# Optimization experiments

Measured on AMD Instinct MI355X. Metric: run time of the kernel, lower is better.

The kernel has to match this reference:

```python
import jax, jax.numpy as jnp
import numpy as np

N = 150000   # nodes
E = 600000   # edges
F_IN = 32    # node features
H = 128      # hidden_channels == MLP_neurons
G = 2048     # graphs in batch


def setup_inputs() -> dict:
    key = jax.random.key(0)
    ks = iter(jax.random.split(key, 40))
    inp = {}
    inp['x'] = jax.random.normal(next(ks), (N, F_IN), dtype=jnp.float32)
    inp['edge_index'] = jax.random.randint(next(ks), (2, E), 0, N)
    inp['batch'] = jnp.sort(jax.random.randint(next(ks), (N,), 0, G))
    # GINConv MLPs: Linear(in,H) ReLU Linear(H,H) ReLU Linear(H,H)
    for i, f_in in enumerate([F_IN, H, H]):
        s1 = 1.0 / np.sqrt(f_in)
        s2 = 1.0 / np.sqrt(H)
        inp[f'c{i}_w1'] = jax.random.uniform(next(ks), (f_in, H), minval=-s1, maxval=s1)
        inp[f'c{i}_b1'] = jnp.zeros((H,), jnp.float32)
        inp[f'c{i}_w2'] = jax.random.uniform(next(ks), (H, H), minval=-s2, maxval=s2)
        inp[f'c{i}_b2'] = jnp.zeros((H,), jnp.float32)
        inp[f'c{i}_w3'] = jax.random.uniform(next(ks), (H, H), minval=-s2, maxval=s2)
        inp[f'c{i}_b3'] = jnp.zeros((H,), jnp.float32)
    s = 1.0 / np.sqrt(H)
    inp['fc0_w'] = jax.random.uniform(next(ks), (H, H), minval=-s, maxval=s)
    inp['fc0_b'] = jnp.zeros((H,), jnp.float32)
    inp['fc1_w'] = jax.random.uniform(next(ks), (H, H), minval=-s, maxval=s)
    inp['fc1_b'] = jnp.zeros((H,), jnp.float32)
    inp['out_w'] = jax.random.uniform(next(ks), (H, 2), minval=-s, maxval=s)
    inp['out_b'] = jnp.zeros((2,), jnp.float32)
    return inp


def _gin_layer(x, edge_index, w1, b1, w2, b2, w3, b3):
    # GINConv with eps=0: h = MLP(x + sum_{j in N(i)} x_j)
    agg = jax.ops.segment_sum(x[edge_index[0]], edge_index[1], num_segments=N)
    h = x + agg
    h = jax.nn.relu(h @ w1 + b1)
    h = jax.nn.relu(h @ w2 + b2)
    h = h @ w3 + b3
    return jax.nn.relu(h)  # outer .relu() in forward


def reference(x, edge_index, batch,
              c0_w1, c0_b1, c0_w2, c0_b2, c0_w3, c0_b3,
              c1_w1, c1_b1, c1_w2, c1_b2, c1_w3, c1_b3,
              c2_w1, c2_b1, c2_w2, c2_b2, c2_w3, c2_b3,
              fc0_w, fc0_b, fc1_w, fc1_b, out_w, out_b):
    h = _gin_layer(x, edge_index, c0_w1, c0_b1, c0_w2, c0_b2, c0_w3, c0_b3)
    h = _gin_layer(h, edge_index, c1_w1, c1_b1, c1_w2, c1_b2, c1_w3, c1_b3)
    h = _gin_layer(h, edge_index, c2_w1, c2_b1, c2_w2, c2_b2, c2_w3, c2_b3)
    # global_mean_pool over graph ids
    sums = jax.ops.segment_sum(h, batch, num_segments=G)            # [G,H]
    cnts = jax.ops.segment_sum(jnp.ones((N,), h.dtype), batch, num_segments=G)
    g = sums / jnp.maximum(cnts, 1.0)[:, None]
    # classifier head (dropout is identity at inference)
    g = jax.nn.relu(g @ fc0_w + fc0_b)
    g = jax.nn.relu(g @ fc1_w + fc1_b)
    return g @ out_w + out_b  # [G,2]
```

## Files before the change

kernel.cpp:

```cpp
#include <hip/hip_runtime.h>
#include <hip/hip_bf16.h>

#define NN 150000
#define EE 600000
#define F_IN 32
#define HD 128
#define GG 2048
#define CAP 28
#define NP 150016

typedef __attribute__((ext_vector_type(8))) short bf16x8;
typedef __attribute__((ext_vector_type(4))) float f32x4;

__device__ inline void split_bf16(float v, unsigned short& hi, unsigned short& lo) {
    __hip_bfloat16 h = __float2bfloat16(v);
    float hv = __bfloat162float(h);
    __hip_bfloat16 l = __float2bfloat16(v - hv);
    hi = *reinterpret_cast<unsigned short*>(&h);
    lo = *reinterpret_cast<unsigned short*>(&l);
}
__device__ inline unsigned short bf16_hi(float v) {
    __hip_bfloat16 h = __float2bfloat16(v);
    return *reinterpret_cast<unsigned short*>(&h);
}
__device__ inline unsigned short bf16_lo(float v) {
    __hip_bfloat16 h = __float2bfloat16(v);
    float hv = __bfloat162float(h);
    __hip_bfloat16 l = __float2bfloat16(v - hv);
    return *reinterpret_cast<unsigned short*>(&l);
}
__device__ inline float bf2f(unsigned short u) {
    union { unsigned int i; float f; } c;
    c.i = ((unsigned int)u) << 16;
    return c.f;
}

__global__ void build_graph(const int* __restrict__ ei,
                            int* __restrict__ cnt_node,
                            int* __restrict__ bucket) {
    int e = blockIdx.x * blockDim.x + threadIdx.x;
    if (e >= EE) return;
    int src = ei[e];
    int dst = ei[EE + e];
    int slot = atomicAdd(&cnt_node[dst], 1);
    if (slot < CAP) bucket[slot * NN + dst] = src;
}

struct PrepDesc { const float* src; unsigned short* dhi; unsigned short* dlo; int K; };
struct PrepArgs { PrepDesc d[9]; };

__global__ void prep_weights(PrepArgs pa) {
    PrepDesc de = pa.d[blockIdx.y];
    int total = de.K * HD;
    int KS = de.K >> 5;
    for (int idx = blockIdx.x * blockDim.x + threadIdx.x; idx < total;
         idx += gridDim.x * blockDim.x) {
        int k = idx / HD, h = idx - (idx / HD) * HD;
        unsigned short hi, lo;
        split_bf16(de.src[idx], hi, lo);
        int nt = h >> 4, m = h & 15;
        int ks = k >> 5, quad = (k >> 3) & 3, e = k & 7;
        int lane = quad * 16 + m;
        int pidx = ((nt * KS + ks) * 64 + lane) * 8 + e;
        de.dhi[pidx] = hi;
        de.dlo[pidx] = lo;
    }
}

template <int K_IN, bool BF16IN, bool POOL>
__launch_bounds__(256, 3)
__global__ void gin_layer(const void* __restrict__ hin_,
                          const int* __restrict__ cnt_node,
                          const int* __restrict__ bucket,
                          const unsigned short* __restrict__ w1h, const unsigned short* __restrict__ w1l,
                          const float* __restrict__ b1,
                          const unsigned short* __restrict__ w2h, const unsigned short* __restrict__ w2l,
                          const float* __restrict__ b2,
                          const unsigned short* __restrict__ w3h, const unsigned short* __restrict__ w3l,
                          const float* __restrict__ b3,
                          unsigned short* __restrict__ out,
                          const int* __restrict__ batch,
                          float* __restrict__ pooled) {
    constexpr int KS1 = K_IN / 32;
    constexpr int UN = BF16IN ? 4 : (KS1 == 1 ? 8 : 2);
    __shared__ unsigned short sh[4][32][HD + 8];

    const int wave = threadIdx.x >> 6;
    const int lane = threadIdx.x & 63;
    const int m = lane & 15;
    const int quad = lane >> 4;
    const int nodeBase = blockIdx.x * 128 + wave * 32;

    const float* hf = (const float*)hin_;
    const unsigned short* hb = (const unsigned short*)hin_;

    bf16x8 ah[2][KS1], al[2][KS1];
#pragma unroll
    for (int s = 0; s < 2; s++) {
        int node = nodeBase + s * 16 + m;
        node = node < NN ? node : NN - 1;
        float ag[KS1][8];
        if (BF16IN) {
            const unsigned short* rs = hb + (size_t)node * K_IN + quad * 8;
#pragma unroll
            for (int ks = 0; ks < KS1; ks++) {
                bf16x8 v = *(const bf16x8*)(rs + ks * 32);
#pragma unroll
                for (int e = 0; e < 8; e++) ag[ks][e] = bf2f((unsigned short)v[e]);
            }
        } else {
            const float* rs = hf + (size_t)node * K_IN + quad * 8;
#pragma unroll
            for (int ks = 0; ks < KS1; ks++) {
                float4 v0 = *(const float4*)(rs + ks * 32);
                float4 v1 = *(const float4*)(rs + ks * 32 + 4);
                ag[ks][0] = v0.x; ag[ks][1] = v0.y; ag[ks][2] = v0.z; ag[ks][3] = v0.w;
                ag[ks][4] = v1.x; ag[ks][5] = v1.y; ag[ks][6] = v1.z; ag[ks][7] = v1.w;
            }
        }
        int cnt = cnt_node[node];
        cnt = cnt < CAP ? cnt : CAP;
        const int* b = bucket + node;
        int i = 0;
        if (BF16IN) {
            for (; i + UN <= cnt; i += UN) {
                bf16x8 v[UN][KS1];
#pragma unroll
                for (int j = 0; j < UN; j++) {
                    const unsigned short* r = hb + (size_t)b[(i + j) * NN] * K_IN + quad * 8;
#pragma unroll
                    for (int ks = 0; ks < KS1; ks++)
                        v[j][ks] = *(const bf16x8*)(r + ks * 32);
                }
#pragma unroll
                for (int ks = 0; ks < KS1; ks++)
#pragma unroll
                    for (int e = 0; e < 8; e++) {
                        float t01 = bf2f((unsigned short)v[0][ks][e]) +
                                    bf2f((unsigned short)v[1][ks][e]);
                        float t23 = bf2f((unsigned short)v[2][ks][e]) +
                                    bf2f((unsigned short)v[3][ks][e]);
                        ag[ks][e] += t01 + t23;
                    }
            }
            for (; i < cnt; i++) {
                const unsigned short* r = hb + (size_t)b[i * NN] * K_IN + quad * 8;
#pragma unroll
                for (int ks = 0; ks < KS1; ks++) {
                    bf16x8 v = *(const bf16x8*)(r + ks * 32);
#pragma unroll
                    for (int e = 0; e < 8; e++) ag[ks][e] += bf2f((unsigned short)v[e]);
                }
            }
        } else {
            for (; i + UN <= cnt; i += UN) {
                float4 v0[UN][KS1], v1[UN][KS1];
#pragma unroll
                for (int j = 0; j < UN; j++) {
                    const float* r = hf + (size_t)b[(i + j) * NN] * K_IN + quad * 8;
#pragma unroll
                    for (int ks = 0; ks < KS1; ks++) {
                        v0[j][ks] = *(const float4*)(r + ks * 32);
                        v1[j][ks] = *(const float4*)(r + ks * 32 + 4);
                    }
                }
#pragma unroll
                for (int ks = 0; ks < KS1; ks++) {
#pragma unroll
                    for (int e = 0; e < 4; e++) {
                        float s01 = (&v0[0][ks].x)[e] + (&v0[1][ks].x)[e];
                        float s23 = (&v0[2][ks].x)[e] + (&v0[3][ks].x)[e];
                        if (UN == 8) {
                            s01 += (&v0[4][ks].x)[e] + (&v0[5][ks].x)[e];
                            s23 += (&v0[6][ks].x)[e] + (&v0[7][ks].x)[e];
                        }
                        ag[ks][e] += s01 + s23;
                    }
#pragma unroll
                    for (int e = 0; e < 4; e++) {
                        float s01 = (&v1[0][ks].x)[e] + (&v1[1][ks].x)[e];
                        float s23 = (&v1[2][ks].x)[e] + (&v1[3][ks].x)[e];
                        if (UN == 8) {
                            s01 += (&v1[4][ks].x)[e] + (&v1[5][ks].x)[e];
                            s23 += (&v1[6][ks].x)[e] + (&v1[7][ks].x)[e];
                        }
                        ag[ks][e + 4] += s01 + s23;
                    }
                }
            }
            for (; i < cnt; i++) {
                const float* r = hf + (size_t)b[i * NN] * K_IN + quad * 8;
#pragma unroll
                for (int ks = 0; ks < KS1; ks++) {
                    float4 v0 = *(const float4*)(r + ks * 32);
                    float4 v1 = *(const float4*)(r + ks * 32 + 4);
                    ag[ks][0] += v0.x; ag[ks][1] += v0.y; ag[ks][2] += v0.z; ag[ks][3] += v0.w;
                    ag[ks][4] += v1.x; ag[ks][5] += v1.y; ag[ks][6] += v1.z; ag[ks][7] += v1.w;
                }
            }
        }
#pragma unroll
        for (int ks = 0; ks < KS1; ks++) {
            bf16x8 vh, vl;
#pragma unroll
            for (int e = 0; e < 8; e++) {
                unsigned short hi, lo;
                split_bf16(ag[ks][e], hi, lo);
                vh[e] = (short)hi;
                vl[e] = (short)lo;
            }
            ah[s][ks] = vh;
            al[s][ks] = vl;
        }
    }

    f32x4 acc[2][8];

#pragma unroll
    for (int nt = 0; nt < 8; nt++) {
        bf16x8 bh[KS1], bl[KS1];
#pragma unroll
        for (int ks = 0; ks < KS1; ks++) {
            bh[ks] = *(const bf16x8*)(w1h + ((nt * KS1 + ks) * 64 + lane) * 8);
            bl[ks] = *(const bf16x8*)(w1l + ((nt * KS1 + ks) * 64 + lane) * 8);
        }
        f32x4 c0 = {0.f, 0.f, 0.f, 0.f};
        f32x4 c1 = {0.f, 0.f, 0.f, 0.f};
#pragma unroll
        for (int ks = 0; ks < KS1; ks++) {
            c0 = __builtin_amdgcn_mfma_f32_16x16x32_bf16(ah[0][ks], bh[ks], c0, 0, 0, 0);
            c1 = __builtin_amdgcn_mfma_f32_16x16x32_bf16(ah[1][ks], bh[ks], c1, 0, 0, 0);
            c0 = __builtin_amdgcn_mfma_f32_16x16x32_bf16(al[0][ks], bh[ks], c0, 0, 0, 0);
            c1 = __builtin_amdgcn_mfma_f32_16x16x32_bf16(al[1][ks], bh[ks], c1, 0, 0, 0);
            c0 = __builtin_amdgcn_mfma_f32_16x16x32_bf16(ah[0][ks], bl[ks], c0, 0, 0, 0);
            c1 = __builtin_amdgcn_mfma_f32_16x16x32_bf16(ah[1][ks], bl[ks], c1, 0, 0, 0);
        }
        acc[0][nt] = c0;
        acc[1][nt] = c1;
    }

    bf16x8 a2h[2][4], a2l[2][4];
#pragma unroll
    for (int s = 0; s < 2; s++)
#pragma unroll
        for (int nt = 0; nt < 8; nt++) {
            float bj = b1[nt * 16 + m];
#pragma unroll
            for (int r = 0; r < 4; r++)
                sh[wave][s * 16 + quad * 4 + r][nt * 16 + m] =
                    bf16_hi(fmaxf(acc[s][nt][r] + bj, 0.f));
        }
#pragma unroll
    for (int s = 0; s < 2; s++)
#pragma unroll
        for (int ks = 0; ks < 4; ks++)
            a2h[s][ks] = *(const bf16x8*)&sh[wave][s * 16 + m][ks * 32 + quad * 8];
#pragma unroll
    for (int s = 0; s < 2; s++)
#pragma unroll
        for (int nt = 0; nt < 8; nt++) {
            float bj = b1[nt * 16 + m];
#pragma unroll
            for (int r = 0; r < 4; r++)
                sh[wave][s * 16 + quad * 4 + r][nt * 16 + m] =
                    bf16_lo(fmaxf(acc[s][nt][r] + bj, 0.f));
        }
#pragma unroll
    for (int s = 0; s < 2; s++)
#pragma unroll
        for (int ks = 0; ks < 4; ks++)
            a2l[s][ks] = *(const bf16x8*)&sh[wave][s * 16 + m][ks * 32 + quad * 8];

#pragma unroll
    for (int nt = 0; nt < 8; nt++) {
        bf16x8 bh[4], bl[4];
#pragma unroll
        for (int ks = 0; ks < 4; ks++) {
            bh[ks] = *(const bf16x8*)(w2h + ((nt * 4 + ks) * 64 + lane) * 8);
            bl[ks] = *(const bf16x8*)(w2l + ((nt * 4 + ks) * 64 + lane) * 8);
        }
        f32x4 c0 = {0.f, 0.f, 0.f, 0.f};
        f32x4 c1 = {0.f, 0.f, 0.f, 0.f};
#pragma unroll
        for (int ks = 0; ks < 4; ks++) {
            c0 = __builtin_amdgcn_mfma_f32_16x16x32_bf16(a2h[0][ks], bh[ks], c0, 0, 0, 0);
            c1 = __builtin_amdgcn_mfma_f32_16x16x32_bf16(a2h[1][ks], bh[ks], c1, 0, 0, 0);
            c0 = __builtin_amdgcn_mfma_f32_16x16x32_bf16(a2l[0][ks], bh[ks], c0, 0, 0, 0);
            c1 = __builtin_amdgcn_mfma_f32_16x16x32_bf16(a2l[1][ks], bh[ks], c1, 0, 0, 0);
            c0 = __builtin_amdgcn_mfma_f32_16x16x32_bf16(a2h[0][ks], bl[ks], c0, 0, 0, 0);
            c1 = __builtin_amdgcn_mfma_f32_16x16x32_bf16(a2h[1][ks], bl[ks], c1, 0, 0, 0);
        }
        acc[0][nt] = c0;
        acc[1][nt] = c1;
    }

#pragma unroll
    for (int s = 0; s < 2; s++)
#pragma unroll
        for (int nt = 0; nt < 8; nt++) {
            float bj = b2[nt * 16 + m];
#pragma unroll
            for (int r = 0; r < 4; r++)
                sh[wave][s * 16 + quad * 4 + r][nt * 16 + m] =
                    bf16_hi(fmaxf(acc[s][nt][r] + bj, 0.f));
        }
#pragma unroll
    for (int s = 0; s < 2; s++)
#pragma unroll
        for (int ks = 0; ks < 4; ks++)
            a2h[s][ks] = *(const bf16x8*)&sh[wave][s * 16 + m][ks * 32 + quad * 8];
#pragma unroll
    for (int s = 0; s < 2; s++)
#pragma unroll
        for (int nt = 0; nt < 8; nt++) {
            float bj = b2[nt * 16 + m];
#pragma unroll
            for (int r = 0; r < 4; r++)
                sh[wave][s * 16 + quad * 4 + r][nt * 16 + m] =
                    bf16_lo(fmaxf(acc[s][nt][r] + bj, 0.f));
        }
#pragma unroll
    for (int s = 0; s < 2; s++)
#pragma unroll
        for (int ks = 0; ks < 4; ks++)
            a2l[s][ks] = *(const bf16x8*)&sh[wave][s * 16 + m][ks * 32 + quad * 8];

#pragma unroll
    for (int nt = 0; nt < 8; nt++) {
        bf16x8 bh[4], bl[4];
#pragma unroll
        for (int ks = 0; ks < 4; ks++) {
            bh[ks] = *(const bf16x8*)(w3h + ((nt * 4 + ks) * 64 + lane) * 8);
            bl[ks] = *(const bf16x8*)(w3l + ((nt * 4 + ks) * 64 + lane) * 8);
        }
        f32x4 c0 = {0.f, 0.f, 0.f, 0.f};
        f32x4 c1 = {0.f, 0.f, 0.f, 0.f};
#pragma unroll
        for (int ks = 0; ks < 4; ks++) {
            c0 = __builtin_amdgcn_mfma_f32_16x16x32_bf16(a2h[0][ks], bh[ks], c0, 0, 0, 0);
            c1 = __builtin_amdgcn_mfma_f32_16x16x32_bf16(a2h[1][ks], bh[ks], c1, 0, 0, 0);
            c0 = __builtin_amdgcn_mfma_f32_16x16x32_bf16(a2l[0][ks], bh[ks], c0, 0, 0, 0);
            c1 = __builtin_amdgcn_mfma_f32_16x16x32_bf16(a2l[1][ks], bh[ks], c1, 0, 0, 0);
            c0 = __builtin_amdgcn_mfma_f32_16x16x32_bf16(a2h[0][ks], bl[ks], c0, 0, 0, 0);
            c1 = __builtin_amdgcn_mfma_f32_16x16x32_bf16(a2h[1][ks], bl[ks], c1, 0, 0, 0);
        }
        acc[0][nt] = c0;
        acc[1][nt] = c1;
    }

    if (POOL) {
        float* shf = (float*)&sh[wave][0][0];
#pragma unroll
        for (int h = 0; h < 2; h++) {
#pragma unroll
            for (int nt = 0; nt < 8; nt++) {
                float bj = b3[nt * 16 + m];
#pragma unroll
                for (int r = 0; r < 4; r++)
                    shf[(quad * 4 + r) * 132 + nt * 16 + m] =
                        fmaxf(acc[h][nt][r] + bj, 0.f);
            }
            int c0 = lane * 2;
            float run0 = 0.f, run1 = 0.f;
            int gp = -1;
            for (int rrow = 0; rrow < 16; rrow++) {
                int node = nodeBase + h * 16 + rrow;
                if (node >= NN) break;
                int g = batch[node];
                float2 xv = *(const float2*)&shf[rrow * 132 + c0];
                if (g != gp) {
                    if (gp >= 0) {
                        atomicAdd(&pooled[(size_t)gp * HD + c0 + 0], run0);
                        atomicAdd(&pooled[(size_t)gp * HD + c0 + 1], run1);
                    }
                    run0 = xv.x; run1 = xv.y; gp = g;
                } else {
                    run0 += xv.x; run1 += xv.y;
                }
            }
            if (gp >= 0) {
                atomicAdd(&pooled[(size_t)gp * HD + c0 + 0], run0);
                atomicAdd(&pooled[(size_t)gp * HD + c0 + 1], run1);
            }
        }
    } else {
#pragma unroll
        for (int s = 0; s < 2; s++)
#pragma unroll
            for (int nt = 0; nt < 8; nt++) {
                float bj = b3[nt * 16 + m];
#pragma unroll
                for (int r = 0; r < 4; r++)
                    sh[wave][s * 16 + quad * 4 + r][nt * 16 + m] =
                        bf16_hi(fmaxf(acc[s][nt][r] + bj, 0.f));
            }
#pragma unroll
        for (int io = 0; io < 8; io++) {
            int row32 = io * 4 + quad;
            int col = m * 8;
            int n2 = nodeBase + row32;
            bf16x8 v = *(const bf16x8*)&sh[wave][row32][col];
            if (n2 < NN) *(bf16x8*)&out[(size_t)n2 * HD + col] = v;
        }
    }
}

__device__ inline int lb_batch(const int* __restrict__ batch, int key) {
    int lo = 0, hi = NN;
    while (lo < hi) {
        int mid = (lo + hi) >> 1;
        if (batch[mid] < key) lo = mid + 1; else hi = mid;
    }
    return lo;
}

__launch_bounds__(128)
__global__ void head(const float* __restrict__ pooled, const int* __restrict__ batch,
                     const float* __restrict__ fc0_w, const float* __restrict__ fc0_b,
                     const float* __restrict__ fc1_w, const float* __restrict__ fc1_b,
                     const float* __restrict__ out_w, const float* __restrict__ out_b,
                     float* __restrict__ out) {
    int g = blockIdx.x;
    int j = threadIdx.x;
    __shared__ float s0[HD];
    __shared__ float s1[HD];
    int c = lb_batch(batch, g + 1) - lb_batch(batch, g);
    float cf = (float)(c > 1 ? c : 1);
    s0[j] = pooled[(size_t)g * HD + j] / cf;
    __syncthreads();

    float acc = fc0_b[j];
    for (int k = 0; k < HD; k += 4) {
        float4 hv = *(const float4*)&s0[k];
        acc = fmaf(hv.x, fc0_w[(k + 0) * HD + j], acc);
        acc = fmaf(hv.y, fc0_w[(k + 1) * HD + j], acc);
        acc = fmaf(hv.z, fc0_w[(k + 2) * HD + j], acc);
        acc = fmaf(hv.w, fc0_w[(k + 3) * HD + j], acc);
    }
    s1[j] = fmaxf(acc, 0.0f);
    __syncthreads();

    acc = fc1_b[j];
    for (int k = 0; k < HD; k += 4) {
        float4 hv = *(const float4*)&s1[k];
        acc = fmaf(hv.x, fc1_w[(k + 0) * HD + j], acc);
        acc = fmaf(hv.y, fc1_w[(k + 1) * HD + j], acc);
        acc = fmaf(hv.z, fc1_w[(k + 2) * HD + j], acc);
        acc = fmaf(hv.w, fc1_w[(k + 3) * HD + j], acc);
    }
    float v = fmaxf(acc, 0.0f);

    float p0 = v * out_w[j * 2 + 0];
    float p1 = v * out_w[j * 2 + 1];
    __syncthreads();
    s0[j] = p0;
    s1[j] = p1;
    __syncthreads();
    for (int off = 64; off >= 1; off >>= 1) {
        if (j < off) {
            s0[j] += s0[j + off];
            s1[j] += s1[j + off];
        }
        __syncthreads();
    }
    if (j == 0) {
        out[(size_t)g * 2 + 0] = s0[0] + out_b[0];
        out[(size_t)g * 2 + 1] = s1[0] + out_b[1];
    }
}

extern "C" void kernel_launch(void* const* d_in, const int* in_sizes, int n_in,
                              void* d_out, int out_size, void* d_ws, size_t ws_size,
                              hipStream_t stream) {
    const float* x     = (const float*)d_in[0];
    const int*   ei    = (const int*)d_in[1];
    const int*   batch = (const int*)d_in[2];
    const float* cw[3][6];
    for (int i = 0; i < 3; i++)
        for (int k = 0; k < 6; k++) cw[i][k] = (const float*)d_in[3 + 6 * i + k];
    const float* fc0_w = (const float*)d_in[21];
    const float* fc0_b = (const float*)d_in[22];
    const float* fc1_w = (const float*)d_in[23];
    const float* fc1_b = (const float*)d_in[24];
    const float* out_w = (const float*)d_in[25];
    const float* out_b = (const float*)d_in[26];
    float* out = (float*)d_out;

    char* ws = (char*)d_ws;
    size_t off = 0;
    auto carve = [&](size_t bytes) {
        void* p = ws + off;
        off += (bytes + 255) & ~(size_t)255;
        return p;
    };
    int*   cnt_node = (int*)carve((size_t)NN * 4);
    float* pooled   = (float*)carve((size_t)GG * HD * 4);
    int*   bucket   = (int*)carve((size_t)NN * CAP * 4);
    unsigned short* hA = (unsigned short*)carve((size_t)NP * HD * 2);
    unsigned short* hB = (unsigned short*)carve((size_t)NP * HD * 2);
    unsigned short* wHi[9];
    unsigned short* wLo[9];
    int wK[9] = {F_IN, HD, HD, HD, HD, HD, HD, HD, HD};
    for (int i = 0; i < 9; i++) {
        wHi[i] = (unsigned short*)carve((size_t)wK[i] * HD * 2);
        wLo[i] = (unsigned short*)carve((size_t)wK[i] * HD * 2);
    }
    (void)ws_size;

    hipMemsetAsync(cnt_node, 0, (size_t)((char*)bucket - (char*)cnt_node), stream);
    build_graph<<<(EE + 255) / 256, 256, 0, stream>>>(ei, cnt_node, bucket);

    PrepArgs pa;
    for (int l = 0; l < 3; l++)
        for (int s = 0; s < 3; s++) {
            int i = l * 3 + s;
            pa.d[i].src = cw[l][2 * s];
            pa.d[i].dhi = wHi[i];
            pa.d[i].dlo = wLo[i];
            pa.d[i].K = wK[i];
        }
    prep_weights<<<dim3(16, 9), 256, 0, stream>>>(pa);

    const int blocks = NP / 128;

    gin_layer<F_IN, false, false><<<blocks, 256, 0, stream>>>(x, cnt_node, bucket,
        wHi[0], wLo[0], cw[0][1], wHi[1], wLo[1], cw[0][3], wHi[2], wLo[2], cw[0][5],
        hA, batch, pooled);
    gin_layer<HD, true, false><<<blocks, 256, 0, stream>>>(hA, cnt_node, bucket,
        wHi[3], wLo[3], cw[1][1], wHi[4], wLo[4], cw[1][3], wHi[5], wLo[5], cw[1][5],
        hB, batch, pooled);
    gin_layer<HD, true, true><<<blocks, 256, 0, stream>>>(hB, cnt_node, bucket,
        wHi[6], wLo[6], cw[2][1], wHi[7], wLo[7], cw[2][3], wHi[8], wLo[8], cw[2][5],
        nullptr, batch, pooled);

    head<<<GG, 128, 0, stream>>>(pooled, batch, fc0_w, fc0_b, fc1_w, fc1_b, out_w, out_b, out);
}
```

Baseline: 520.5 us.

## Split neighbor aggregation into separate wave-per-node-group kernels before MLP

Each GIN layer becomes two kernels. A dedicated aggregation kernel has one wave handle four nodes, with lanes spread across feature dimensions and neighbor indices broadcast by shuffle. It writes the summed features as hi/lo bf16 planes that the MLP kernel reads directly. The bucket layout changes to node-major so a node's neighbor list is contiguous, and the memset is replaced by a zeroing kernel. This trades the fused kernel's poorly coalesced per-lane gather and low occupancy for extra global round trips of the aggregated tensors and more launches.

```diff
diff --git a/kernel.cpp b/kernel.cpp
--- a/kernel.cpp
+++ b/kernel.cpp
@@ -33,6 +33,17 @@
     union { unsigned int i; float f; } c;
     c.i = ((unsigned int)u) << 16;
     return c.f;
+}
+__device__ inline float asfloat(unsigned int u) {
+    union { unsigned int i; float f; } c;
+    c.i = u;
+    return c.f;
+}
+
+__global__ void init_zero(int* __restrict__ cnt_node, float* __restrict__ pooled) {
+    int i = blockIdx.x * blockDim.x + threadIdx.x;
+    if (i < NN) cnt_node[i] = 0;
+    if (i < GG * HD) pooled[i] = 0.f;
 }
 
 __global__ void build_graph(const int* __restrict__ ei,
@@ -43,7 +54,7 @@
     int src = ei[e];
     int dst = ei[EE + e];
     int slot = atomicAdd(&cnt_node[dst], 1);
-    if (slot < CAP) bucket[slot * NN + dst] = src;
+    if (slot < CAP) bucket[dst * CAP + slot] = src;
 }
 
 struct PrepDesc { const float* src; unsigned short* dhi; unsigned short* dlo; int K; };
@@ -67,22 +78,157 @@
     }
 }
 
-template <int K_IN, bool BF16IN, bool POOL>
-__launch_bounds__(256, 3)
-__global__ void gin_layer(const void* __restrict__ hin_,
-                          const int* __restrict__ cnt_node,
-                          const int* __restrict__ bucket,
-                          const unsigned short* __restrict__ w1h, const unsigned short* __restrict__ w1l,
-                          const float* __restrict__ b1,
-                          const unsigned short* __restrict__ w2h, const unsigned short* __restrict__ w2l,
-                          const float* __restrict__ b2,
-                          const unsigned short* __restrict__ w3h, const unsigned short* __restrict__ w3l,
-                          const float* __restrict__ b3,
-                          unsigned short* __restrict__ out,
-                          const int* __restrict__ batch,
-                          float* __restrict__ pooled) {
+__launch_bounds__(256, 8)
+__global__ void agg_b16(const unsigned short* __restrict__ hb,
+                        const int* __restrict__ cnt_node,
+                        const int* __restrict__ bucket,
+                        unsigned short* __restrict__ aggH,
+                        unsigned short* __restrict__ aggL) {
+    const int wave = threadIdx.x >> 6;
+    const int lane = threadIdx.x & 63;
+    const int nbase = (blockIdx.x * 4 + wave) * 4;
+    if (nbase >= NN) return;
+
+    int cv = cnt_node[min(nbase + (lane & 3), NN - 1)];
+    int tots[4];
+#pragma unroll
+    for (int i = 0; i < 4; i++) {
+        int c = __shfl(cv, i);
+        c = c < CAP ? c : CAP;
+        tots[i] = (nbase + i < NN) ? c + 1 : 0;
+    }
+    int idxv[4];
+#pragma unroll
+    for (int i = 0; i < 4; i++) {
+        int n = min(nbase + i, NN - 1);
+        int slot = (lane >= 1 && lane <= CAP) ? lane - 1 : 0;
+        int bv = bucket[n * CAP + slot];
+        idxv[i] = (lane == 0) ? n : bv;
+    }
+    int mtot = max(max(tots[0], tots[1]), max(tots[2], tots[3]));
+
+    float a0[4] = {0.f, 0.f, 0.f, 0.f};
+    float a1[4] = {0.f, 0.f, 0.f, 0.f};
+
+    int j = 0;
+    while (j < mtot) {
+        unsigned int v[4][2];
+#pragma unroll
+        for (int i = 0; i < 4; i++)
+#pragma unroll
+            for (int jj = 0; jj < 2; jj++) {
+                v[i][jj] = 0u;
+                if (j + jj < tots[i]) {
+                    int sidx = __shfl(idxv[i], j + jj);
+                    v[i][jj] = *(const unsigned int*)(hb + (size_t)sidx * HD + lane * 2);
+                }
+            }
+#pragma unroll
+        for (int i = 0; i < 4; i++)
+#pragma unroll
+            for (int jj = 0; jj < 2; jj++) {
+                a0[i] += asfloat(v[i][jj] << 16);
+                a1[i] += asfloat(v[i][jj] & 0xffff0000u);
+            }
+        j += 2;
+    }
+
+#pragma unroll
+    for (int i = 0; i < 4; i++) {
+        if (nbase + i >= NN) break;
+        unsigned short h0, l0, h1, l1;
+        split_bf16(a0[i], h0, l0);
+        split_bf16(a1[i], h1, l1);
+        unsigned int ph = (unsigned int)h0 | ((unsigned int)h1 << 16);
+        unsigned int pl = (unsigned int)l0 | ((unsigned int)l1 << 16);
+        *(unsigned int*)(aggH + (size_t)(nbase + i) * HD + lane * 2) = ph;
+        *(unsigned int*)(aggL + (size_t)(nbase + i) * HD + lane * 2) = pl;
+    }
+}
+
+__launch_bounds__(256, 8)
+__global__ void agg_f32(const float* __restrict__ x,
+                        const int* __restrict__ cnt_node,
+                        const int* __restrict__ bucket,
+                        unsigned short* __restrict__ aggH,
+                        unsigned short* __restrict__ aggL) {
+    const int wave = threadIdx.x >> 6;
+    const int lane = threadIdx.x & 63;
+    const int half = lane >> 5;
+    const int dim = lane & 31;
+    const int nbase = (blockIdx.x * 4 + wave) * 4;
+    if (nbase >= NN) return;
+
+    int cv = cnt_node[min(nbase + (lane & 3), NN - 1)];
+    int tots[4];
+#pragma unroll
+    for (int i = 0; i < 4; i++) {
+        int c = __shfl(cv, i);
+        c = c < CAP ? c : CAP;
+        tots[i] = (nbase + i < NN) ? c + 1 : 0;
+    }
+    int idxv[4];
+#pragma unroll
+    for (int i = 0; i < 4; i++) {
+        int n = min(nbase + i, NN - 1);
+        int slot = (lane >= 1 && lane <= CAP) ? lane - 1 : 0;
+        int bv = bucket[n * CAP + slot];
+        idxv[i] = (lane == 0) ? n : bv;
+    }
+    int mtot = max(max(tots[0], tots[1]), max(tots[2], tots[3]));
+
+    float a[4] = {0.f, 0.f, 0.f, 0.f};
+
+    int j = 0;
+    while (j < mtot) {
+        float v[4][2], w[4][2];
+#pragma unroll
+        for (int i = 0; i < 4; i++)
+#pragma unroll
+            for (int p = 0; p < 2; p++) {
+                v[i][p] = 0.f; w[i][p] = 0.f;
+                int jb = j + p * 2;
+                if (jb < tots[i]) {
+                    int jj = jb + half;
+                    bool ok = jj < tots[i];
+                    int sidx = __shfl(idxv[i], ok ? jj : jb);
+                    v[i][p] = x[(size_t)sidx * F_IN + dim];
+                    w[i][p] = ok ? 1.f : 0.f;
+                }
+            }
+#pragma unroll
+        for (int i = 0; i < 4; i++)
+#pragma unroll
+            for (int p = 0; p < 2; p++)
+                a[i] = fmaf(v[i][p], w[i][p], a[i]);
+        j += 4;
+    }
+#pragma unroll
+    for (int i = 0; i < 4; i++) a[i] += __shfl_xor(a[i], 32);
+
+#pragma unroll
+    for (int i = 0; i < 4; i++) {
+        if (nbase + i >= NN) break;
+        unsigned short outv = half ? bf16_lo(a[i]) : bf16_hi(a[i]);
+        unsigned short* p = (half ? aggL : aggH) + (size_t)(nbase + i) * F_IN + dim;
+        *p = outv;
+    }
+}
+
+template <int K_IN, bool POOL>
+__launch_bounds__(256, 4)
+__global__ void gin_mlp(const unsigned short* __restrict__ aggH,
+                        const unsigned short* __restrict__ aggL,
+                        const unsigned short* __restrict__ w1h, const unsigned short* __restrict__ w1l,
+                        const float* __restrict__ b1,
+                        const unsigned short* __restrict__ w2h, const unsigned short* __restrict__ w2l,
+                        const float* __restrict__ b2,
+                        const unsigned short* __restrict__ w3h, const unsigned short* __restrict__ w3l,
+                        const float* __restrict__ b3,
+                        unsigned short* __restrict__ out,
+                        const int* __restrict__ batch,
+                        float* __restrict__ pooled) {
     constexpr int KS1 = K_IN / 32;
-    constexpr int UN = BF16IN ? 4 : (KS1 == 1 ? 8 : 2);
     __shared__ unsigned short sh[4][32][HD + 8];
 
     const int wave = threadIdx.x >> 6;
@@ -91,126 +237,17 @@
     const int quad = lane >> 4;
     const int nodeBase = blockIdx.x * 128 + wave * 32;
 
-    const float* hf = (const float*)hin_;
-    const unsigned short* hb = (const unsigned short*)hin_;
-
     bf16x8 ah[2][KS1], al[2][KS1];
 #pragma unroll
     for (int s = 0; s < 2; s++) {
         int node = nodeBase + s * 16 + m;
         node = node < NN ? node : NN - 1;
-        float ag[KS1][8];
-        if (BF16IN) {
-            const unsigned short* rs = hb + (size_t)node * K_IN + quad * 8;
-#pragma unroll
-            for (int ks = 0; ks < KS1; ks++) {
-                bf16x8 v = *(const bf16x8*)(rs + ks * 32);
-#pragma unroll
-                for (int e = 0; e < 8; e++) ag[ks][e] = bf2f((unsigned short)v[e]);
-            }
-        } else {
-            const float* rs = hf + (size_t)node * K_IN + quad * 8;
-#pragma unroll
-            for (int ks = 0; ks < KS1; ks++) {
-                float4 v0 = *(const float4*)(rs + ks * 32);
-                float4 v1 = *(const float4*)(rs + ks * 32 + 4);
-                ag[ks][0] = v0.x; ag[ks][1] = v0.y; ag[ks][2] = v0.z; ag[ks][3] = v0.w;
-                ag[ks][4] = v1.x; ag[ks][5] = v1.y; ag[ks][6] = v1.z; ag[ks][7] = v1.w;
-            }
-        }
-        int cnt = cnt_node[node];
-        cnt = cnt < CAP ? cnt : CAP;
-        const int* b = bucket + node;
-        int i = 0;
-        if (BF16IN) {
-            for (; i + UN <= cnt; i += UN) {
-                bf16x8 v[UN][KS1];
-#pragma unroll
-                for (int j = 0; j < UN; j++) {
-                    const unsigned short* r = hb + (size_t)b[(i + j) * NN] * K_IN + quad * 8;
-#pragma unroll
-                    for (int ks = 0; ks < KS1; ks++)
-                        v[j][ks] = *(const bf16x8*)(r + ks * 32);
-                }
-#pragma unroll
-                for (int ks = 0; ks < KS1; ks++)
-#pragma unroll
-                    for (int e = 0; e < 8; e++) {
-                        float t01 = bf2f((unsigned short)v[0][ks][e]) +
-                                    bf2f((unsigned short)v[1][ks][e]);
-                        float t23 = bf2f((unsigned short)v[2][ks][e]) +
-                                    bf2f((unsigned short)v[3][ks][e]);
-                        ag[ks][e] += t01 + t23;
-                    }
-            }
-            for (; i < cnt; i++) {
-                const unsigned short* r = hb + (size_t)b[i * NN] * K_IN + quad * 8;
-#pragma unroll
-                for (int ks = 0; ks < KS1; ks++) {
-                    bf16x8 v = *(const bf16x8*)(r + ks * 32);
-#pragma unroll
-                    for (int e = 0; e < 8; e++) ag[ks][e] += bf2f((unsigned short)v[e]);
-                }
-            }
-        } else {
-            for (; i + UN <= cnt; i += UN) {
-                float4 v0[UN][KS1], v1[UN][KS1];
-#pragma unroll
-                for (int j = 0; j < UN; j++) {
-                    const float* r = hf + (size_t)b[(i + j) * NN] * K_IN + quad * 8;
-#pragma unroll
-                    for (int ks = 0; ks < KS1; ks++) {
-                        v0[j][ks] = *(const float4*)(r + ks * 32);
-                        v1[j][ks] = *(const float4*)(r + ks * 32 + 4);
-                    }
-                }
-#pragma unroll
-                for (int ks = 0; ks < KS1; ks++) {
-#pragma unroll
-                    for (int e = 0; e < 4; e++) {
-                        float s01 = (&v0[0][ks].x)[e] + (&v0[1][ks].x)[e];
-                        float s23 = (&v0[2][ks].x)[e] + (&v0[3][ks].x)[e];
-                        if (UN == 8) {
-                            s01 += (&v0[4][ks].x)[e] + (&v0[5][ks].x)[e];
-                            s23 += (&v0[6][ks].x)[e] + (&v0[7][ks].x)[e];
-                        }
-                        ag[ks][e] += s01 + s23;
-                    }
-#pragma unroll
-                    for (int e = 0; e < 4; e++) {
-                        float s01 = (&v1[0][ks].x)[e] + (&v1[1][ks].x)[e];
-                        float s23 = (&v1[2][ks].x)[e] + (&v1[3][ks].x)[e];
-                        if (UN == 8) {
-                            s01 += (&v1[4][ks].x)[e] + (&v1[5][ks].x)[e];
-                            s23 += (&v1[6][ks].x)[e] + (&v1[7][ks].x)[e];
-                        }
-                        ag[ks][e + 4] += s01 + s23;
-                    }
-                }
-            }
-            for (; i < cnt; i++) {
-                const float* r = hf + (size_t)b[i * NN] * K_IN + quad * 8;
-#pragma unroll
-                for (int ks = 0; ks < KS1; ks++) {
-                    float4 v0 = *(const float4*)(r + ks * 32);
-                    float4 v1 = *(const float4*)(r + ks * 32 + 4);
-                    ag[ks][0] += v0.x; ag[ks][1] += v0.y; ag[ks][2] += v0.z; ag[ks][3] += v0.w;
-                    ag[ks][4] += v1.x; ag[ks][5] += v1.y; ag[ks][6] += v1.z; ag[ks][7] += v1.w;
-                }
-            }
-        }
+        const unsigned short* rh = aggH + (size_t)node * K_IN + quad * 8;
+        const unsigned short* rl = aggL + (size_t)node * K_IN + quad * 8;
 #pragma unroll
         for (int ks = 0; ks < KS1; ks++) {
-            bf16x8 vh, vl;
-#pragma unroll
-            for (int e = 0; e < 8; e++) {
-                unsigned short hi, lo;
-                split_bf16(ag[ks][e], hi, lo);
-                vh[e] = (short)hi;
-                vl[e] = (short)lo;
-            }
-            ah[s][ks] = vh;
-            al[s][ks] = vl;
+            ah[s][ks] = *(const bf16x8*)(rh + ks * 32);
+            al[s][ks] = *(const bf16x8*)(rl + ks * 32);
         }
     }
 
@@ -495,9 +532,11 @@
     };
     int*   cnt_node = (int*)carve((size_t)NN * 4);
     float* pooled   = (float*)carve((size_t)GG * HD * 4);
-    int*   bucket   = (int*)carve((size_t)NN * CAP * 4);
-    unsigned short* hA = (unsigned short*)carve((size_t)NP * HD * 2);
-    unsigned short* hB = (unsigned short*)carve((size_t)NP * HD * 2);
+    int*   bucket   = (int*)carve((size_t)NN * CAP * 4 + 256);
+    unsigned short* hA   = (unsigned short*)carve((size_t)NP * HD * 2);
+    unsigned short* hB   = (unsigned short*)carve((size_t)NP * HD * 2);
+    unsigned short* aggH = (unsigned short*)carve((size_t)NP * HD * 2);
+    unsigned short* aggL = (unsigned short*)carve((size_t)NP * HD * 2);
     unsigned short* wHi[9];
     unsigned short* wLo[9];
     int wK[9] = {F_IN, HD, HD, HD, HD, HD, HD, HD, HD};
@@ -507,7 +546,7 @@
     }
     (void)ws_size;
 
-    hipMemsetAsync(cnt_node, 0, (size_t)((char*)bucket - (char*)cnt_node), stream);
+    init_zero<<<(GG * HD + 255) / 256, 256, 0, stream>>>(cnt_node, pooled);
     build_graph<<<(EE + 255) / 256, 256, 0, stream>>>(ei, cnt_node, bucket);
 
     PrepArgs pa;
@@ -522,14 +561,18 @@
     prep_weights<<<dim3(16, 9), 256, 0, stream>>>(pa);
 
     const int blocks = NP / 128;
-
-    gin_layer<F_IN, false, false><<<blocks, 256, 0, stream>>>(x, cnt_node, bucket,
+    const int ablocks = (NN + 15) / 16;
+
+    agg_f32<<<ablocks, 256, 0, stream>>>(x, cnt_node, bucket, aggH, aggL);
+    gin_mlp<F_IN, false><<<blocks, 256, 0, stream>>>(aggH, aggL,
         wHi[0], wLo[0], cw[0][1], wHi[1], wLo[1], cw[0][3], wHi[2], wLo[2], cw[0][5],
         hA, batch, pooled);
-    gin_layer<HD, true, false><<<blocks, 256, 0, stream>>>(hA, cnt_node, bucket,
+    agg_b16<<<ablocks, 256, 0, stream>>>(hA, cnt_node, bucket, aggH, aggL);
+    gin_mlp<HD, false><<<blocks, 256, 0, stream>>>(aggH, aggL,
         wHi[3], wLo[3], cw[1][1], wHi[4], wLo[4], cw[1][3], wHi[5], wLo[5], cw[1][5],
         hB, batch, pooled);
-    gin_layer<HD, true, true><<<blocks, 256, 0, stream>>>(hB, cnt_node, bucket,
+    agg_b16<<<ablocks, 256, 0, stream>>>(hB, cnt_node, bucket, aggH, aggL);
+    gin_mlp<HD, true><<<blocks, 256, 0, stream>>>(aggH, aggL,
         wHi[6], wLo[6], cw[2][1], wHi[7], wLo[7], cw[2][3], wHi[8], wLo[8], cw[2][5],
         nullptr, batch, pooled);
 
```

After: 617.6 us. 1.19x slower.

## Make neighbor buckets node-major and pack hi/lo bf16 splits in one LDS pass

Applied to the files above, without the earlier changes.

The neighbor bucket layout changes from slot-major to node-major (dst*CAP+slot), so each node's neighbor list sits in contiguous memory instead of being strided by NN. The hidden-activation hi/lo bf16 split now happens once, packed into 32-bit LDS words, and is unpacked with byte-permute instructions, replacing two separate LDS round trips. Each pass handles one 16-row half at a time, which shrinks the shared tile. The memset is also replaced by a small zero-init kernel. Within a node, loads become contiguous, but adjacent lanes now read bucket entries CAP ints apart, which reduces coalescing on the index loads.

```diff
diff --git a/kernel.cpp b/kernel.cpp
--- a/kernel.cpp
+++ b/kernel.cpp
@@ -23,16 +23,16 @@
     __hip_bfloat16 h = __float2bfloat16(v);
     return *reinterpret_cast<unsigned short*>(&h);
 }
-__device__ inline unsigned short bf16_lo(float v) {
-    __hip_bfloat16 h = __float2bfloat16(v);
-    float hv = __bfloat162float(h);
-    __hip_bfloat16 l = __float2bfloat16(v - hv);
-    return *reinterpret_cast<unsigned short*>(&l);
-}
 __device__ inline float bf2f(unsigned short u) {
     union { unsigned int i; float f; } c;
     c.i = ((unsigned int)u) << 16;
     return c.f;
+}
+
+__global__ void init_zero(int* __restrict__ cnt_node, float* __restrict__ pooled) {
+    int i = blockIdx.x * blockDim.x + threadIdx.x;
+    if (i < NN) cnt_node[i] = 0;
+    if (i < GG * HD) pooled[i] = 0.f;
 }
 
 __global__ void build_graph(const int* __restrict__ ei,
@@ -43,7 +43,7 @@
     int src = ei[e];
     int dst = ei[EE + e];
     int slot = atomicAdd(&cnt_node[dst], 1);
-    if (slot < CAP) bucket[slot * NN + dst] = src;
+    if (slot < CAP) bucket[dst * CAP + slot] = src;
 }
 
 struct PrepDesc { const float* src; unsigned short* dhi; unsigned short* dlo; int K; };
@@ -83,7 +83,7 @@
                           float* __restrict__ pooled) {
     constexpr int KS1 = K_IN / 32;
     constexpr int UN = BF16IN ? 4 : (KS1 == 1 ? 8 : 2);
-    __shared__ unsigned short sh[4][32][HD + 8];
+    __shared__ unsigned int shp[4][16][132];
 
     const int wave = threadIdx.x >> 6;
     const int lane = threadIdx.x & 63;
@@ -120,14 +120,14 @@
         }
         int cnt = cnt_node[node];
         cnt = cnt < CAP ? cnt : CAP;
-        const int* b = bucket + node;
+        const int* b = bucket + (size_t)node * CAP;
         int i = 0;
         if (BF16IN) {
             for (; i + UN <= cnt; i += UN) {
                 bf16x8 v[UN][KS1];
 #pragma unroll
                 for (int j = 0; j < UN; j++) {
-                    const unsigned short* r = hb + (size_t)b[(i + j) * NN] * K_IN + quad * 8;
+                    const unsigned short* r = hb + (size_t)b[i + j] * K_IN + quad * 8;
 #pragma unroll
                     for (int ks = 0; ks < KS1; ks++)
                         v[j][ks] = *(const bf16x8*)(r + ks * 32);
@@ -144,7 +144,7 @@
                     }
             }
             for (; i < cnt; i++) {
-                const unsigned short* r = hb + (size_t)b[i * NN] * K_IN + quad * 8;
+                const unsigned short* r = hb + (size_t)b[i] * K_IN + quad * 8;
 #pragma unroll
                 for (int ks = 0; ks < KS1; ks++) {
                     bf16x8 v = *(const bf16x8*)(r + ks * 32);
@@ -157,7 +157,7 @@
                 float4 v0[UN][KS1], v1[UN][KS1];
 #pragma unroll
                 for (int j = 0; j < UN; j++) {
-                    const float* r = hf + (size_t)b[(i + j) * NN] * K_IN + quad * 8;
+                    const float* r = hf + (size_t)b[i + j] * K_IN + quad * 8;
 #pragma unroll
                     for (int ks = 0; ks < KS1; ks++) {
                         v0[j][ks] = *(const float4*)(r + ks * 32);
@@ -189,7 +189,7 @@
                 }
             }
             for (; i < cnt; i++) {
-                const float* r = hf + (size_t)b[i * NN] * K_IN + quad * 8;
+                const float* r = hf + (size_t)b[i] * K_IN + quad * 8;
 #pragma unroll
                 for (int ks = 0; ks < KS1; ks++) {
                     float4 v0 = *(const float4*)(r + ks * 32);
@@ -241,35 +241,36 @@
 
     bf16x8 a2h[2][4], a2l[2][4];
 #pragma unroll
-    for (int s = 0; s < 2; s++)
+    for (int s = 0; s < 2; s++) {
 #pragma unroll
         for (int nt = 0; nt < 8; nt++) {
             float bj = b1[nt * 16 + m];
 #pragma unroll
-            for (int r = 0; r < 4; r++)
-                sh[wave][s * 16 + quad * 4 + r][nt * 16 + m] =
-                    bf16_hi(fmaxf(acc[s][nt][r] + bj, 0.f));
-        }
-#pragma unroll
-    for (int s = 0; s < 2; s++)
-#pragma unroll
-        for (int ks = 0; ks < 4; ks++)
-            a2h[s][ks] = *(const bf16x8*)&sh[wave][s * 16 + m][ks * 32 + quad * 8];
-#pragma unroll
-    for (int s = 0; s < 2; s++)
-#pragma unroll
-        for (int nt = 0; nt < 8; nt++) {
-            float bj = b1[nt * 16 + m];
-#pragma unroll
-            for (int r = 0; r < 4; r++)
-                sh[wave][s * 16 + quad * 4 + r][nt * 16 + m] =
-                    bf16_lo(fmaxf(acc[s][nt][r] + bj, 0.f));
-        }
-#pragma unroll
-    for (int s = 0; s < 2; s++)
-#pragma unroll
-        for (int ks = 0; ks < 4; ks++)
-            a2l[s][ks] = *(const bf16x8*)&sh[wave][s * 16 + m][ks * 32 + quad * 8];
+            for (int r = 0; r < 4; r++) {
+                unsigned short hi, lo;
+                split_bf16(fmaxf(acc[s][nt][r] + bj, 0.f), hi, lo);
+                shp[wave][quad * 4 + r][nt * 16 + m] =
+                    (unsigned int)hi | ((unsigned int)lo << 16);
+            }
+        }
+#pragma unroll
+        for (int ks = 0; ks < 4; ks++) {
+            const unsigned int* rp = &shp[wave][m][ks * 32 + quad * 8];
+            uint4 wa = *(const uint4*)rp;
+            uint4 wb = *(const uint4*)(rp + 4);
+            union { unsigned int u[4]; bf16x8 v; } ch, cl;
+            ch.u[0] = __builtin_amdgcn_perm(wa.y, wa.x, 0x05040100u);
+            ch.u[1] = __builtin_amdgcn_perm(wa.w, wa.z, 0x05040100u);
+            ch.u[2] = __builtin_amdgcn_perm(wb.y, wb.x, 0x05040100u);
+            ch.u[3] = __builtin_amdgcn_perm(wb.w, wb.z, 0x05040100u);
+            cl.u[0] = __builtin_amdgcn_perm(wa.y, wa.x, 0x07060302u);
+            cl.u[1] = __builtin_amdgcn_perm(wa.w, wa.z, 0x07060302u);
+            cl.u[2] = __builtin_amdgcn_perm(wb.y, wb.x, 0x07060302u);
+            cl.u[3] = __builtin_amdgcn_perm(wb.w, wb.z, 0x07060302u);
+            a2h[s][ks] = ch.v;
+            a2l[s][ks] = cl.v;
+        }
+    }
 
 #pragma unroll
     for (int nt = 0; nt < 8; nt++) {
@@ -295,35 +296,36 @@
     }
 
 #pragma unroll
-    for (int s = 0; s < 2; s++)
+    for (int s = 0; s < 2; s++) {
 #pragma unroll
         for (int nt = 0; nt < 8; nt++) {
             float bj = b2[nt * 16 + m];
 #pragma unroll
-            for (int r = 0; r < 4; r++)
-                sh[wave][s * 16 + quad * 4 + r][nt * 16 + m] =
-                    bf16_hi(fmaxf(acc[s][nt][r] + bj, 0.f));
-        }
-#pragma unroll
-    for (int s = 0; s < 2; s++)
-#pragma unroll
-        for (int ks = 0; ks < 4; ks++)
-            a2h[s][ks] = *(const bf16x8*)&sh[wave][s * 16 + m][ks * 32 + quad * 8];
-#pragma unroll
-    for (int s = 0; s < 2; s++)
-#pragma unroll
-        for (int nt = 0; nt < 8; nt++) {
-            float bj = b2[nt * 16 + m];
-#pragma unroll
-            for (int r = 0; r < 4; r++)
-                sh[wave][s * 16 + quad * 4 + r][nt * 16 + m] =
-                    bf16_lo(fmaxf(acc[s][nt][r] + bj, 0.f));
-        }
-#pragma unroll
-    for (int s = 0; s < 2; s++)
-#pragma unroll
-        for (int ks = 0; ks < 4; ks++)
-            a2l[s][ks] = *(const bf16x8*)&sh[wave][s * 16 + m][ks * 32 + quad * 8];
+            for (int r = 0; r < 4; r++) {
+                unsigned short hi, lo;
+                split_bf16(fmaxf(acc[s][nt][r] + bj, 0.f), hi, lo);
+                shp[wave][quad * 4 + r][nt * 16 + m] =
+                    (unsigned int)hi | ((unsigned int)lo << 16);
+            }
+        }
+#pragma unroll
+        for (int ks = 0; ks < 4; ks++) {
+            const unsigned int* rp = &shp[wave][m][ks * 32 + quad * 8];
+            uint4 wa = *(const uint4*)rp;
+            uint4 wb = *(const uint4*)(rp + 4);
+            union { unsigned int u[4]; bf16x8 v; } ch, cl;
+            ch.u[0] = __builtin_amdgcn_perm(wa.y, wa.x, 0x05040100u);
+            ch.u[1] = __builtin_amdgcn_perm(wa.w, wa.z, 0x05040100u);
+            ch.u[2] = __builtin_amdgcn_perm(wb.y, wb.x, 0x05040100u);
+            ch.u[3] = __builtin_amdgcn_perm(wb.w, wb.z, 0x05040100u);
+            cl.u[0] = __builtin_amdgcn_perm(wa.y, wa.x, 0x07060302u);
+            cl.u[1] = __builtin_amdgcn_perm(wa.w, wa.z, 0x07060302u);
+            cl.u[2] = __builtin_amdgcn_perm(wb.y, wb.x, 0x07060302u);
+            cl.u[3] = __builtin_amdgcn_perm(wb.w, wb.z, 0x07060302u);
+            a2h[s][ks] = ch.v;
+            a2l[s][ks] = cl.v;
+        }
+    }
 
 #pragma unroll
     for (int nt = 0; nt < 8; nt++) {
@@ -349,7 +351,7 @@
     }
 
     if (POOL) {
-        float* shf = (float*)&sh[wave][0][0];
+        float* shf = (float*)&shp[wave][0][0];
 #pragma unroll
         for (int h = 0; h < 2; h++) {
 #pragma unroll
@@ -384,23 +386,25 @@
             }
         }
     } else {
-#pragma unroll
-        for (int s = 0; s < 2; s++)
+        unsigned short* sh16 = (unsigned short*)&shp[wave][0][0];
+#pragma unroll
+        for (int s = 0; s < 2; s++) {
 #pragma unroll
             for (int nt = 0; nt < 8; nt++) {
                 float bj = b3[nt * 16 + m];
 #pragma unroll
                 for (int r = 0; r < 4; r++)
-                    sh[wave][s * 16 + quad * 4 + r][nt * 16 + m] =
+                    sh16[(quad * 4 + r) * 264 + nt * 16 + m] =
                         bf16_hi(fmaxf(acc[s][nt][r] + bj, 0.f));
             }
 #pragma unroll
-        for (int io = 0; io < 8; io++) {
-            int row32 = io * 4 + quad;
-            int col = m * 8;
-            int n2 = nodeBase + row32;
-            bf16x8 v = *(const bf16x8*)&sh[wave][row32][col];
-            if (n2 < NN) *(bf16x8*)&out[(size_t)n2 * HD + col] = v;
+            for (int io = 0; io < 4; io++) {
+                int row16 = io * 4 + quad;
+                int col = m * 8;
+                int n2 = nodeBase + s * 16 + row16;
+                bf16x8 v = *(const bf16x8*)&sh16[row16 * 264 + col];
+                if (n2 < NN) *(bf16x8*)&out[(size_t)n2 * HD + col] = v;
+            }
         }
     }
 }
@@ -507,7 +511,7 @@
     }
     (void)ws_size;
 
-    hipMemsetAsync(cnt_node, 0, (size_t)((char*)bucket - (char*)cnt_node), stream);
+    init_zero<<<(GG * HD + 255) / 256, 256, 0, stream>>>(cnt_node, pooled);
     build_graph<<<(EE + 255) / 256, 256, 0, stream>>>(ei, cnt_node, bucket);
 
     PrepArgs pa;
```

New measurement: 499.7 us. 4.0% less time.
